# Kernel optimization log

Hardware: AMD Instinct MI355X
Metric: run time of the kernel (lower is better)

Reference implementation:

```python
import jax, jax.numpy as jnp
from jax import lax
import numpy as np

HIDDEN = 256
UID_EMB, LOC_EMB, WD_EMB, HR_EMB = 64, 128, 16, 16
UID_NUM, LOC_NUM = 5000, 50000
S, L, C = 32, 32, 128   # steps, current-trace prefix length, candidates per step
HN, LH = 32, 64         # history traces, history trace length
EMB = UID_EMB + LOC_EMB + WD_EMB + HR_EMB  # 224


def setup_inputs() -> dict:
    key = jax.random.key(0)
    ks = jax.random.split(key, 20)
    def lin(k, o, i, s=0.05):
        return jax.random.normal(k, (o, i), jnp.float32) * s
    return {
        "uid": 7,
        "current_trace": jnp.stack([
            jax.random.randint(ks[0], (S, L), 0, LOC_NUM),
            jax.random.randint(ks[1], (S, L), 0, 7),
            jax.random.randint(ks[2], (S, L), 0, 24)], axis=-1),
        "history_trace": jnp.stack([
            jax.random.randint(ks[3], (HN, LH), 0, LOC_NUM),
            jax.random.randint(ks[4], (HN, LH), 0, 7),
            jax.random.randint(ks[5], (HN, LH), 0, 24)], axis=-1),
        "candidate_set": jax.random.randint(ks[6], (S, C), 0, LOC_NUM),
        "uid_emb": jax.random.normal(ks[7], (UID_NUM, UID_EMB), jnp.float32),
        "loc_emb": jax.random.normal(ks[8], (LOC_NUM, LOC_EMB), jnp.float32),
        "weekday_emb": jax.random.normal(ks[9], (7, WD_EMB), jnp.float32),
        "hour_emb": jax.random.normal(ks[10], (24, HR_EMB), jnp.float32),
        "W_ih": lin(ks[11], 3 * HIDDEN, EMB),
        "W_hh": lin(ks[12], 3 * HIDDEN, HIDDEN),
        "b_ih": jnp.zeros((3 * HIDDEN,), jnp.float32),
        "b_hh": jnp.zeros((3 * HIDDEN,), jnp.float32),
        "intra_w1": lin(ks[13], HIDDEN, HIDDEN),
        "intra_w2": lin(ks[14], HIDDEN, HIDDEN),
        "intra_out": lin(ks[15], 1, HIDDEN),
        "inter_w1": lin(ks[16], HIDDEN, HIDDEN),
        "inter_w2": lin(ks[17], HIDDEN, HIDDEN),
        "inter_out": lin(ks[18], 1, HIDDEN),
        "score_w": lin(ks[19], 1, HIDDEN),
    }


def _gru(x, W_ih, W_hh, b_ih, b_hh):
    # x: [B, T, D] -> all hidden states [B, T, H]; single-layer torch GRU equations
    B = x.shape[0]
    H = W_hh.shape[1]
    x_proj = x @ W_ih.T + b_ih  # [B, T, 3H], precomputed input projection
    def step(h, xp):
        gh = h @ W_hh.T + b_hh
        xr, xz, xn = jnp.split(xp, 3, axis=-1)
        hr, hz, hn = jnp.split(gh, 3, axis=-1)
        r = jax.nn.sigmoid(xr + hr)
        z = jax.nn.sigmoid(xz + hz)
        n = jnp.tanh(xn + r * hn)
        h_new = (1.0 - z) * n + z * h
        return h_new, h_new
    h0 = jnp.zeros((B, H), x.dtype)
    _, hs = lax.scan(step, h0, jnp.swapaxes(x_proj, 0, 1))
    return jnp.swapaxes(hs, 0, 1)


def _forward(uid, current_trace, history_trace, candidate_set,
             uid_emb, loc_emb, weekday_emb, hour_emb,
             W_ih, W_hh, b_ih, b_hh,
             intra_w1, intra_w2, intra_out,
             inter_w1, inter_w2, inter_out, score_w):
    def encode(trace):  # [B, T, 3] int -> [B, H]
        B, T, _ = trace.shape
        u = jnp.broadcast_to(uid_emb[uid][None, None, :], (B, T, UID_EMB))
        e = jnp.concatenate([u,
                             loc_emb[trace[:, :, 0]],
                             weekday_emb[trace[:, :, 1]],
                             hour_emb[trace[:, :, 2]]], axis=-1)
        hs = _gru(e, W_ih, W_hh, b_ih, b_hh)
        # intra-trajectory attention: query = last hidden state, key = all hidden states
        qh = jax.nn.relu(hs[:, -1, :] @ intra_w1.T)[:, None, :]
        kh = jax.nn.relu(hs @ intra_w2.T)
        a = (jnp.tanh(qh + kh) @ intra_out.T)[..., 0]  # [B, T]
        w = jax.nn.softmax(a, axis=1)
        return jnp.einsum('bt,bth->bh', w, hs)

    hist_hidden = encode(history_trace)  # [HN, H]

    S_, L_, _ = current_trace.shape
    C_ = candidate_set.shape[1]
    last_time = current_trace[:, -1, 1:3]  # [S, 2] weekday/hour of last observed point
    cand_point = jnp.concatenate(
        [candidate_set[..., None],
         jnp.broadcast_to(last_time[:, None, :], (S_, C_, 2))], axis=-1)  # [S, C, 3]
    cand_trace = jnp.concatenate(
        [jnp.broadcast_to(current_trace[:, None], (S_, C_, L_, 3)),
         cand_point[:, :, None, :]], axis=2)  # [S, C, L+1, 3]
    cand_hidden = encode(cand_trace.reshape(S_ * C_, L_ + 1, 3))  # [S*C, H]

    # inter-trajectory attention; history key is shared across all candidates
    qh = jax.nn.relu(cand_hidden @ inter_w1.T)      # [S*C, H]
    kh = jax.nn.relu(hist_hidden @ inter_w2.T)      # [HN, H]
    a = (jnp.tanh(qh[:, None, :] + kh[None]) @ inter_out.T)[..., 0]  # [S*C, HN]
    w = jax.nn.softmax(a, axis=1)
    moving = w @ hist_hidden                        # [S*C, H]

    scores = (moving @ score_w.T)[:, 0].reshape(S_, C_)
    probs = jax.nn.softmax(scores, axis=1)          # softmax over candidate set per step
    return probs, moving.reshape(S_, C_, HIDDEN)


def reference(uid, current_trace, history_trace, candidate_set,
              uid_emb, loc_emb, weekday_emb, hour_emb,
              W_ih, W_hh, b_ih, b_hh,
              intra_w1, intra_w2, intra_out,
              inter_w1, inter_w2, inter_out, score_w):
    return _forward(uid, current_trace, history_trace, candidate_set,
                    uid_emb, loc_emb, weekday_emb, hour_emb,
                    W_ih, W_hh, b_ih, b_hh,
                    intra_w1, intra_w2, intra_out,
                    inter_w1, inter_w2, inter_out, score_w)
```

## Files before the change

### kernel.cpp

```cpp
#include <hip/hip_runtime.h>
#include <math.h>

#define NHID   256
#define NEMB   224

constexpr int OFF_BASE = 0;
constexpr int OFF_WDP  = 768;
constexpr int OFF_HRP  = OFF_WDP + 7*768;
constexpr int OFF_XPH  = OFF_HRP + 24*768;
constexpr int OFF_XPC  = OFF_XPH + 32*64*768;
constexpr int OFF_HSH  = OFF_XPC + 32*32*768;
constexpr int OFF_HSC  = OFF_HSH + 32*64*256;
constexpr int OFF_GHL  = OFF_HSC + 32*32*256;
constexpr int OFF_QHH  = OFF_GHL + 32*768;
constexpr int OFF_HC   = OFF_QHH + 32*256;
constexpr int OFF_KHH  = OFF_HC  + 4096*256;
constexpr int OFF_KHSH = OFF_KHH + 32*64*256;
constexpr int OFF_KHC  = OFF_KHSH+ 32*32*256;
constexpr int OFF_QHC  = OFF_KHC + 4096*256;
constexpr int OFF_HIST = OFF_QHC + 4096*256;
constexpr int OFF_CHID = OFF_HIST+ 32*256;
constexpr int OFF_QH2  = OFF_CHID+ 4096*256;
constexpr int OFF_KH2  = OFF_QH2 + 4096*256;
constexpr int OFF_SC   = OFF_KH2 + 32*256;
constexpr int OFF_W16  = OFF_KHH;

__device__ __forceinline__ float sigm(float x) { return 1.0f / (1.0f + __expf(-x)); }

typedef _Float16 half2_t __attribute__((ext_vector_type(2)));

__device__ __forceinline__ float fdot2f(unsigned int a, unsigned int b, float c) {
#if __has_builtin(__builtin_amdgcn_fdot2)
  return __builtin_amdgcn_fdot2(__builtin_bit_cast(half2_t, a),
                                __builtin_bit_cast(half2_t, b), c, false);
#else
  half2_t x = __builtin_bit_cast(half2_t, a);
  half2_t y = __builtin_bit_cast(half2_t, b);
  return c + (float)x[0] * (float)y[0] + (float)x[1] * (float)y[1];
#endif
}

__device__ __forceinline__ unsigned int packh(float a, float b) {
  unsigned short lo = __builtin_bit_cast(unsigned short, (_Float16)a);
  unsigned short hi = __builtin_bit_cast(unsigned short, (_Float16)b);
  return (unsigned int)lo | ((unsigned int)hi << 16);
}

__global__ __launch_bounds__(256) void k_prep(const int* uid, const float* uid_emb,
                                              const float* wde, const float* hre,
                                              const float* W_ih, const float* b_ih,
                                              float* ws) {
  __shared__ __align__(16) float ev[64];
  int blk = blockIdx.x, tid = threadIdx.x;
  if (blk == 0) {
    if (tid < 64) ev[tid] = uid_emb[uid[0] * 64 + tid];
    __syncthreads();
    #pragma unroll
    for (int jj = 0; jj < 3; ++jj) {
      int j = tid + jj * 256;
      float acc = b_ih[j];
      const float* wr = W_ih + j * NEMB;
      #pragma unroll
      for (int k = 0; k < 64; k += 4) {
        float4 w = *(const float4*)(wr + k);
        acc += ev[k]*w.x + ev[k+1]*w.y + ev[k+2]*w.z + ev[k+3]*w.w;
      }
      ws[OFF_BASE + j] = acc;
    }
  } else if (blk < 8) {
    int wd = blk - 1;
    if (tid < 16) ev[tid] = wde[wd * 16 + tid];
    __syncthreads();
    #pragma unroll
    for (int jj = 0; jj < 3; ++jj) {
      int j = tid + jj * 256;
      float acc = 0.f;
      const float* wr = W_ih + j * NEMB + 192;
      #pragma unroll
      for (int k = 0; k < 16; k += 4) {
        float4 w = *(const float4*)(wr + k);
        acc += ev[k]*w.x + ev[k+1]*w.y + ev[k+2]*w.z + ev[k+3]*w.w;
      }
      ws[OFF_WDP + wd * 768 + j] = acc;
    }
  } else {
    int hr = blk - 8;
    if (tid < 16) ev[tid] = hre[hr * 16 + tid];
    __syncthreads();
    #pragma unroll
    for (int jj = 0; jj < 3; ++jj) {
      int j = tid + jj * 256;
      float acc = 0.f;
      const float* wr = W_ih + j * NEMB + 208;
      #pragma unroll
      for (int k = 0; k < 16; k += 4) {
        float4 w = *(const float4*)(wr + k);
        acc += ev[k]*w.x + ev[k+1]*w.y + ev[k+2]*w.z + ev[k+3]*w.w;
      }
      ws[OFF_HRP + hr * 768 + j] = acc;
    }
  }
}

__global__ __launch_bounds__(256) void k_pack(const float* W_hh, float* ws) {
  int idx = blockIdx.x * 256 + threadIdx.x;
  int i4 = idx & 31, j = idx >> 5;
  const float4* p = (const float4*)(W_hh + j * 256 + i4 * 8);
  float4 a = p[0], b = p[1];
  uint4 o;
  o.x = packh(a.x, a.y); o.y = packh(a.z, a.w);
  o.z = packh(b.x, b.y); o.w = packh(b.z, b.w);
  ((uint4*)((unsigned int*)ws + OFF_W16))[i4 * 768 + j] = o;
}

__global__ __launch_bounds__(256) void k_xproj(const int* cur_tr, const int* hist_tr,
                                               const float* loc_emb, const float* W_ih,
                                               float* ws) {
  __shared__ float Ws[768][17];
  __shared__ float Xs[16][20];
  __shared__ int s_wd[16], s_hr[16], s_loc[16];
  int blk = blockIdx.x, tid = threadIdx.x;
  int r0 = blk * 16;

  if (tid < 16) {
    int row = r0 + tid;
    const int* tr; int idx;
    if (row < 2048) { tr = hist_tr; idx = row; } else { tr = cur_tr; idx = row - 2048; }
    s_loc[tid] = tr[idx * 3];
    s_wd[tid]  = tr[idx * 3 + 1];
    s_hr[tid]  = tr[idx * 3 + 2];
  }
  __syncthreads();

  float accA[16], accB[16], accC[16];
  #pragma unroll
  for (int r = 0; r < 16; ++r) { accA[r] = 0.f; accB[r] = 0.f; accC[r] = 0.f; }

  for (int kb = 0; kb < 8; ++kb) {
    for (int i = tid; i < 768 * 4; i += 256) {
      int j = i >> 2, q = (i & 3) * 4;
      float4 w = *(const float4*)&W_ih[j * NEMB + 64 + kb * 16 + q];
      Ws[j][q] = w.x; Ws[j][q+1] = w.y; Ws[j][q+2] = w.z; Ws[j][q+3] = w.w;
    }
    if (tid < 64) {
      int r = tid >> 2, q = (tid & 3) * 4;
      float4 x = *(const float4*)&loc_emb[s_loc[r] * 128 + kb * 16 + q];
      Xs[q][r] = x.x; Xs[q+1][r] = x.y; Xs[q+2][r] = x.z; Xs[q+3][r] = x.w;
    }
    __syncthreads();
    #pragma unroll
    for (int kk = 0; kk < 16; ++kk) {
      float wa = Ws[tid][kk], wb = Ws[tid + 256][kk], wc = Ws[tid + 512][kk];
      float4 x0 = *(const float4*)&Xs[kk][0];
      float4 x1 = *(const float4*)&Xs[kk][4];
      float4 x2 = *(const float4*)&Xs[kk][8];
      float4 x3 = *(const float4*)&Xs[kk][12];
      float xv[16] = {x0.x,x0.y,x0.z,x0.w, x1.x,x1.y,x1.z,x1.w,
                      x2.x,x2.y,x2.z,x2.w, x3.x,x3.y,x3.z,x3.w};
      #pragma unroll
      for (int r = 0; r < 16; ++r) {
        accA[r] += xv[r] * wa; accB[r] += xv[r] * wb; accC[r] += xv[r] * wc;
      }
    }
    __syncthreads();
  }

  float bA = ws[OFF_BASE + tid], bB = ws[OFF_BASE + 256 + tid], bC = ws[OFF_BASE + 512 + tid];
  for (int r = 0; r < 16; ++r) {
    int row = r0 + r;
    float* outp = (row < 2048) ? (ws + OFF_XPH + row * 768)
                               : (ws + OFF_XPC + (row - 2048) * 768);
    const float* wdp = ws + OFF_WDP + s_wd[r] * 768;
    const float* hrp = ws + OFF_HRP + s_hr[r] * 768;
    outp[tid]       = accA[r] + bA + wdp[tid]       + hrp[tid];
    outp[256 + tid] = accB[r] + bB + wdp[256 + tid] + hrp[256 + tid];
    outp[512 + tid] = accC[r] + bC + wdp[512 + tid] + hrp[512 + tid];
  }
}

__global__ __launch_bounds__(768) void k_gru(const float* b_hh, const float* intra_w1,
                                             float* ws) {
  __shared__ __align__(16) float gh[768];
  __shared__ __align__(16) float h32[256];
  __shared__ __align__(16) unsigned short h16[256];
  int w = blockIdx.x, tid = threadIdx.x;
  int T; const float* xp; float* hs;
  if (w < 32) { T = 64; xp = ws + OFF_XPH + w * 64 * 768; hs = ws + OFF_HSH + w * 64 * 256; }
  else        { T = 32; int b = w - 32; xp = ws + OFF_XPC + b * 32 * 768; hs = ws + OFF_HSC + b * 32 * 256; }

  uint4 wreg[32];
  {
    const uint4* wp = (const uint4*)((const unsigned int*)ws + OFF_W16) + tid;
    #pragma unroll
    for (int i = 0; i < 32; ++i) wreg[i] = wp[i * 768];
  }
  float bh = b_hh[tid];
  if (tid < 256) { h32[tid] = 0.f; h16[tid] = 0; }
  __syncthreads();

  for (int t = 0; t < T; ++t) {
    float xr, xz, xn;
    if (tid < 256) {
      xr = xp[t * 768 + tid];
      xz = xp[t * 768 + 256 + tid];
      xn = xp[t * 768 + 512 + tid];
    }
    float acc = bh;
    const uint4* hp = (const uint4*)h16;
    #pragma unroll
    for (int i = 0; i < 32; ++i) {
      uint4 hv = hp[i];
      acc = fdot2f(wreg[i].x, hv.x, acc);
      acc = fdot2f(wreg[i].y, hv.y, acc);
      acc = fdot2f(wreg[i].z, hv.z, acc);
      acc = fdot2f(wreg[i].w, hv.w, acc);
    }
    gh[tid] = acc;
    __syncthreads();
    if (tid < 256) {
      float r  = sigm(xr + gh[tid]);
      float z  = sigm(xz + gh[256 + tid]);
      float n  = tanhf(xn + r * gh[512 + tid]);
      float hn = (1.f - z) * n + z * h32[tid];
      h32[tid] = hn;
      hs[t * 256 + tid] = hn;
      h16[tid] = __builtin_bit_cast(unsigned short, (_Float16)hn);
    }
    __syncthreads();
  }

  if (w < 32) {
    if (tid < 256) {
      float acc = 0.f;
      const float* r1 = intra_w1 + tid * 256;
      #pragma unroll 16
      for (int k = 0; k < 256; k += 4) {
        float4 wv = *(const float4*)(r1 + k);
        float4 hv = *(const float4*)&h32[k];
        acc += hv.x*wv.x + hv.y*wv.y + hv.z*wv.z + hv.w*wv.w;
      }
      ws[OFF_QHH + w * 256 + tid] = fmaxf(acc, 0.f);
    }
  } else {
    float acc = bh;
    const uint4* hp = (const uint4*)h16;
    #pragma unroll
    for (int i = 0; i < 32; ++i) {
      uint4 hv = hp[i];
      acc = fdot2f(wreg[i].x, hv.x, acc);
      acc = fdot2f(wreg[i].y, hv.y, acc);
      acc = fdot2f(wreg[i].z, hv.z, acc);
      acc = fdot2f(wreg[i].w, hv.w, acc);
    }
    ws[OFF_GHL + (w - 32) * 768 + tid] = acc;
  }
}

__global__ __launch_bounds__(256) void k_cand(const int* cur_tr, const int* cand_set,
                                              const float* loc_emb, const float* W_ih,
                                              float* ws) {
  __shared__ float Ws[768][17];
  __shared__ float Xs[16][20];
  int blk = blockIdx.x, tid = threadIdx.x;
  int r0 = blk * 16;
  int s = r0 >> 7;

  float accA[16], accB[16], accC[16];
  #pragma unroll
  for (int r = 0; r < 16; ++r) { accA[r] = 0.f; accB[r] = 0.f; accC[r] = 0.f; }

  for (int kb = 0; kb < 8; ++kb) {
    for (int i = tid; i < 768 * 4; i += 256) {
      int j = i >> 2, q = (i & 3) * 4;
      float4 w = *(const float4*)&W_ih[j * NEMB + 64 + kb * 16 + q];
      Ws[j][q] = w.x; Ws[j][q+1] = w.y; Ws[j][q+2] = w.z; Ws[j][q+3] = w.w;
    }
    if (tid < 64) {
      int r = tid >> 2, q = (tid & 3) * 4;
      float4 x = *(const float4*)&loc_emb[cand_set[r0 + r] * 128 + kb * 16 + q];
      Xs[q][r] = x.x; Xs[q+1][r] = x.y; Xs[q+2][r] = x.z; Xs[q+3][r] = x.w;
    }
    __syncthreads();
    #pragma unroll
    for (int kk = 0; kk < 16; ++kk) {
      float wa = Ws[tid][kk], wb = Ws[tid + 256][kk], wc = Ws[tid + 512][kk];
      float4 x0 = *(const float4*)&Xs[kk][0];
      float4 x1 = *(const float4*)&Xs[kk][4];
      float4 x2 = *(const float4*)&Xs[kk][8];
      float4 x3 = *(const float4*)&Xs[kk][12];
      float xv[16] = {x0.x,x0.y,x0.z,x0.w, x1.x,x1.y,x1.z,x1.w,
                      x2.x,x2.y,x2.z,x2.w, x3.x,x3.y,x3.z,x3.w};
      #pragma unroll
      for (int r = 0; r < 16; ++r) {
        accA[r] += xv[r] * wa; accB[r] += xv[r] * wb; accC[r] += xv[r] * wc;
      }
    }
    __syncthreads();
  }

  int last = s * 32 + 31;
  int wd = cur_tr[last * 3 + 1], hr = cur_tr[last * 3 + 2];
  const float* wdp = ws + OFF_WDP + wd * 768;
  const float* hrp = ws + OFF_HRP + hr * 768;
  float xbA = ws[OFF_BASE + tid]       + wdp[tid]       + hrp[tid];
  float xbB = ws[OFF_BASE + 256 + tid] + wdp[256 + tid] + hrp[256 + tid];
  float xbC = ws[OFF_BASE + 512 + tid] + wdp[512 + tid] + hrp[512 + tid];
  float ghr = ws[OFF_GHL + s * 768 + tid];
  float ghz = ws[OFF_GHL + s * 768 + 256 + tid];
  float ghn = ws[OFF_GHL + s * 768 + 512 + tid];
  float hp  = ws[OFF_HSC + last * 256 + tid];

  for (int r = 0; r < 16; ++r) {
    float rr = sigm(xbA + accA[r] + ghr);
    float zz = sigm(xbB + accB[r] + ghz);
    float nn = tanhf(xbC + accC[r] + ghn);
    float hn = (1.f - zz) * nn + zz * hp;
    ws[OFF_HC + (r0 + r) * 256 + tid] = hn;
  }
}

__device__ __forceinline__ void proj_body(const float* in, float* out, const float* W,
                                          int r0, int tid) {
  __shared__ float Ws[256][33];
  __shared__ float Xs[32][36];
  int c0 = tid & 63, rg = (tid >> 6) * 8;
  float acc[4][8];
  #pragma unroll
  for (int c = 0; c < 4; ++c)
    #pragma unroll
    for (int r = 0; r < 8; ++r) acc[c][r] = 0.f;

  for (int kb = 0; kb < 8; ++kb) {
    for (int i = tid; i < 256 * 8; i += 256) {
      int j = i >> 3, q = (i & 7) * 4;
      float4 v = *(const float4*)&W[j * 256 + kb * 32 + q];
      Ws[j][q] = v.x; Ws[j][q+1] = v.y; Ws[j][q+2] = v.z; Ws[j][q+3] = v.w;
    }
    {
      int r = tid >> 3, q = (tid & 7) * 4;
      float4 v = *(const float4*)&in[(r0 + r) * 256 + kb * 32 + q];
      Xs[q][r] = v.x; Xs[q+1][r] = v.y; Xs[q+2][r] = v.z; Xs[q+3][r] = v.w;
    }
    __syncthreads();
    #pragma unroll
    for (int kk = 0; kk < 32; ++kk) {
      float w0 = Ws[c0][kk], w1 = Ws[c0 + 64][kk], w2 = Ws[c0 + 128][kk], w3 = Ws[c0 + 192][kk];
      float4 xa = *(const float4*)&Xs[kk][rg];
      float4 xb = *(const float4*)&Xs[kk][rg + 4];
      float xv[8] = {xa.x,xa.y,xa.z,xa.w, xb.x,xb.y,xb.z,xb.w};
      #pragma unroll
      for (int r = 0; r < 8; ++r) {
        acc[0][r] += xv[r] * w0; acc[1][r] += xv[r] * w1;
        acc[2][r] += xv[r] * w2; acc[3][r] += xv[r] * w3;
      }
    }
    __syncthreads();
  }
  #pragma unroll
  for (int c = 0; c < 4; ++c)
    for (int r = 0; r < 8; ++r)
      out[(r0 + rg + r) * 256 + c0 + c * 64] = fmaxf(acc[c][r], 0.f);
}

__global__ __launch_bounds__(256) void k_proj_intra(const float* intra_w1, const float* intra_w2,
                                                    float* ws) {
  int blk = blockIdx.x, tid = threadIdx.x;
  const float* in; float* out; const float* W; int r0;
  if (blk < 64)       { in = ws + OFF_HSH; out = ws + OFF_KHH;  W = intra_w2; r0 = blk * 32; }
  else if (blk < 96)  { in = ws + OFF_HSC; out = ws + OFF_KHSH; W = intra_w2; r0 = (blk - 64) * 32; }
  else if (blk < 224) { in = ws + OFF_HC;  out = ws + OFF_KHC;  W = intra_w2; r0 = (blk - 96) * 32; }
  else                { in = ws + OFF_HC;  out = ws + OFF_QHC;  W = intra_w1; r0 = (blk - 224) * 32; }
  proj_body(in, out, W, r0, tid);
}

__global__ __launch_bounds__(256) void k_proj_inter(const float* inter_w1, const float* inter_w2,
                                                    float* ws) {
  int blk = blockIdx.x, tid = threadIdx.x;
  const float* in; float* out; const float* W; int r0;
  if (blk < 128) { in = ws + OFF_CHID; out = ws + OFF_QH2; W = inter_w1; r0 = blk * 32; }
  else           { in = ws + OFF_HIST; out = ws + OFF_KH2; W = inter_w2; r0 = 0; }
  proj_body(in, out, W, r0, tid);
}

__global__ __launch_bounds__(256) void k_hist_attn(const float* intra_out, float* ws) {
  __shared__ __align__(16) float a[64];
  int b = blockIdx.x, tid = threadIdx.x;
  int wv = tid >> 6, lane = tid & 63;
  const float* qh = ws + OFF_QHH + b * 256;
  const float* kh = ws + OFF_KHH + b * 64 * 256;
  const float* hs = ws + OFF_HSH + b * 64 * 256;

  float4 q4  = *(const float4*)&qh[lane * 4];
  float4 io4 = *(const float4*)&intra_out[lane * 4];
  for (int t = wv; t < 64; t += 4) {
    float4 k4 = *(const float4*)&kh[t * 256 + lane * 4];
    float p = tanhf(q4.x + k4.x) * io4.x + tanhf(q4.y + k4.y) * io4.y +
              tanhf(q4.z + k4.z) * io4.z + tanhf(q4.w + k4.w) * io4.w;
    #pragma unroll
    for (int off = 32; off; off >>= 1) p += __shfl_down(p, off);
    if (lane == 0) a[t] = p;
  }
  __syncthreads();
  if (tid < 64) {
    float v = a[tid];
    float m = v;
    #pragma unroll
    for (int off = 32; off; off >>= 1) m = fmaxf(m, __shfl_xor(m, off));
    float e = __expf(v - m);
    float ssum = e;
    #pragma unroll
    for (int off = 32; off; off >>= 1) ssum += __shfl_xor(ssum, off);
    a[tid] = e / ssum;
  }
  __syncthreads();
  float acc = 0.f;
  for (int t = 0; t < 64; ++t) acc += a[t] * hs[t * 256 + tid];
  ws[OFF_HIST + b * 256 + tid] = acc;
}

__global__ __launch_bounds__(64) void k_cand_attn(const float* intra_out, float* ws) {
  int bId = blockIdx.x;
  int s = bId >> 7;
  int lane = threadIdx.x;
  const float* qh  = ws + OFF_QHC  + bId * 256;
  const float* khs = ws + OFF_KHSH + s * 32 * 256;
  const float* khc = ws + OFF_KHC  + bId * 256;
  const float* hsc = ws + OFF_HSC  + s * 32 * 256;
  const float* hc  = ws + OFF_HC   + bId * 256;

  float4 q4  = *(const float4*)&qh[lane * 4];
  float4 io4 = *(const float4*)&intra_out[lane * 4];
  float aa[33];
  float m = -1e30f;
  for (int t = 0; t < 33; ++t) {
    const float* kk = (t < 32) ? &khs[t * 256] : khc;
    float4 k4 = *(const float4*)&kk[lane * 4];
    float p = tanhf(q4.x + k4.x) * io4.x + tanhf(q4.y + k4.y) * io4.y +
              tanhf(q4.z + k4.z) * io4.z + tanhf(q4.w + k4.w) * io4.w;
    #pragma unroll
    for (int off = 32; off; off >>= 1) p += __shfl_xor(p, off);
    aa[t] = p;
    m = fmaxf(m, p);
  }
  float ssum = 0.f;
  #pragma unroll
  for (int t = 0; t < 33; ++t) { aa[t] = __expf(aa[t] - m); ssum += aa[t]; }
  float inv = 1.f / ssum;
  float ax = 0.f, ay = 0.f, az = 0.f, aw = 0.f;
  for (int t = 0; t < 32; ++t) {
    float wt = aa[t] * inv;
    float4 hv = *(const float4*)&hsc[t * 256 + lane * 4];
    ax += wt * hv.x; ay += wt * hv.y; az += wt * hv.z; aw += wt * hv.w;
  }
  {
    float wt = aa[32] * inv;
    float4 hv = *(const float4*)&hc[lane * 4];
    ax += wt * hv.x; ay += wt * hv.y; az += wt * hv.z; aw += wt * hv.w;
  }
  float4 o; o.x = ax; o.y = ay; o.z = az; o.w = aw;
  *(float4*)&ws[OFF_CHID + bId * 256 + lane * 4] = o;
}

__global__ __launch_bounds__(64) void k_inter_attn(const float* inter_out, const float* score_w,
                                                   float* ws, float* d_out) {
  int bId = blockIdx.x;
  int lane = threadIdx.x;
  const float* qh   = ws + OFF_QH2 + bId * 256;
  const float* kh2  = ws + OFF_KH2;
  const float* hist = ws + OFF_HIST;

  float4 q4  = *(const float4*)&qh[lane * 4];
  float4 io4 = *(const float4*)&inter_out[lane * 4];
  float aa[32];
  float m = -1e30f;
  for (int t = 0; t < 32; ++t) {
    float4 k4 = *(const float4*)&kh2[t * 256 + lane * 4];
    float p = tanhf(q4.x + k4.x) * io4.x + tanhf(q4.y + k4.y) * io4.y +
              tanhf(q4.z + k4.z) * io4.z + tanhf(q4.w + k4.w) * io4.w;
    #pragma unroll
    for (int off = 32; off; off >>= 1) p += __shfl_xor(p, off);
    aa[t] = p;
    m = fmaxf(m, p);
  }
  float ssum = 0.f;
  #pragma unroll
  for (int t = 0; t < 32; ++t) { aa[t] = __expf(aa[t] - m); ssum += aa[t]; }
  float inv = 1.f / ssum;
  float ax = 0.f, ay = 0.f, az = 0.f, aw = 0.f;
  for (int t = 0; t < 32; ++t) {
    float wt = aa[t] * inv;
    float4 hv = *(const float4*)&hist[t * 256 + lane * 4];
    ax += wt * hv.x; ay += wt * hv.y; az += wt * hv.z; aw += wt * hv.w;
  }
  float4 o; o.x = ax; o.y = ay; o.z = az; o.w = aw;
  *(float4*)&d_out[4096 + bId * 256 + lane * 4] = o;
  float4 sw = *(const float4*)&score_w[lane * 4];
  float sc = ax*sw.x + ay*sw.y + az*sw.z + aw*sw.w;
  #pragma unroll
  for (int off = 32; off; off >>= 1) sc += __shfl_xor(sc, off);
  if (lane == 0) ws[OFF_SC + bId] = sc;
}

__global__ __launch_bounds__(64) void k_probs(const float* ws, float* d_out) {
  int s = blockIdx.x, lane = threadIdx.x;
  float v0 = ws[OFF_SC + s * 128 + lane];
  float v1 = ws[OFF_SC + s * 128 + 64 + lane];
  float m = fmaxf(v0, v1);
  #pragma unroll
  for (int off = 32; off; off >>= 1) m = fmaxf(m, __shfl_xor(m, off));
  float e0 = __expf(v0 - m), e1 = __expf(v1 - m);
  float ssum = e0 + e1;
  #pragma unroll
  for (int off = 32; off; off >>= 1) ssum += __shfl_xor(ssum, off);
  float inv = 1.f / ssum;
  d_out[s * 128 + lane] = e0 * inv;
  d_out[s * 128 + 64 + lane] = e1 * inv;
}

extern "C" void kernel_launch(void* const* d_in, const int* in_sizes, int n_in,
                              void* d_out, int out_size, void* d_ws, size_t ws_size,
                              hipStream_t stream) {
  const int*   uid      = (const int*)  d_in[0];
  const int*   cur_tr   = (const int*)  d_in[1];
  const int*   hist_tr  = (const int*)  d_in[2];
  const int*   cand_set = (const int*)  d_in[3];
  const float* uid_emb  = (const float*)d_in[4];
  const float* loc_emb  = (const float*)d_in[5];
  const float* wde      = (const float*)d_in[6];
  const float* hre      = (const float*)d_in[7];
  const float* W_ih     = (const float*)d_in[8];
  const float* W_hh     = (const float*)d_in[9];
  const float* b_ih     = (const float*)d_in[10];
  const float* b_hh     = (const float*)d_in[11];
  const float* intra_w1 = (const float*)d_in[12];
  const float* intra_w2 = (const float*)d_in[13];
  const float* intra_out= (const float*)d_in[14];
  const float* inter_w1 = (const float*)d_in[15];
  const float* inter_w2 = (const float*)d_in[16];
  const float* inter_out= (const float*)d_in[17];
  const float* score_w  = (const float*)d_in[18];
  float* ws  = (float*)d_ws;
  float* out = (float*)d_out;

  hipLaunchKernelGGL(k_prep,       dim3(32),   dim3(256), 0, stream, uid, uid_emb, wde, hre, W_ih, b_ih, ws);
  hipLaunchKernelGGL(k_pack,       dim3(96),   dim3(256), 0, stream, W_hh, ws);
  hipLaunchKernelGGL(k_xproj,      dim3(192),  dim3(256), 0, stream, cur_tr, hist_tr, loc_emb, W_ih, ws);
  hipLaunchKernelGGL(k_gru,        dim3(64),   dim3(768), 0, stream, b_hh, intra_w1, ws);
  hipLaunchKernelGGL(k_cand,       dim3(256),  dim3(256), 0, stream, cur_tr, cand_set, loc_emb, W_ih, ws);
  hipLaunchKernelGGL(k_proj_intra, dim3(352),  dim3(256), 0, stream, intra_w1, intra_w2, ws);
  hipLaunchKernelGGL(k_hist_attn,  dim3(32),   dim3(256), 0, stream, intra_out, ws);
  hipLaunchKernelGGL(k_cand_attn,  dim3(4096), dim3(64),  0, stream, intra_out, ws);
  hipLaunchKernelGGL(k_proj_inter, dim3(129),  dim3(256), 0, stream, inter_w1, inter_w2, ws);
  hipLaunchKernelGGL(k_inter_attn, dim3(4096), dim3(64),  0, stream, inter_out, score_w, ws, out);
  hipLaunchKernelGGL(k_probs,      dim3(32),   dim3(64),  0, stream, ws, out);
}
```

Before: 454.9 us.

## Restructure attention kernels to per-lane keys, fast tanh, merge pack into prep

The two candidate attention kernels now process four candidates per 256-thread block. The shared keys, queries and output weights are staged in LDS, and each lane computes one full attention score by itself instead of doing a wave-wide shuffle reduction for every key. tanhf is replaced by an exp-based fast approximation throughout, including the GRU recurrence. The W_hh fp16 pack kernel is folded into k_prep as extra blocks, removing one launch. In exchange there are per-lane serial 256-long loops, heavy LDS traffic, and possible accuracy loss from the fast tanh.

Result: faster. 440.5 us (-3.1%).

```diff
diff --git a/kernel.cpp b/kernel.cpp
--- a/kernel.cpp
+++ b/kernel.cpp
@@ -26,6 +26,9 @@
 constexpr int OFF_W16  = OFF_KHH;
 
 __device__ __forceinline__ float sigm(float x) { return 1.0f / (1.0f + __expf(-x)); }
+__device__ __forceinline__ float tanhf_fast(float x) {
+  return 1.f - 2.f / (__expf(2.f * x) + 1.f);
+}
 
 typedef _Float16 half2_t __attribute__((ext_vector_type(2)));
 
@@ -49,9 +52,20 @@
 __global__ __launch_bounds__(256) void k_prep(const int* uid, const float* uid_emb,
                                               const float* wde, const float* hre,
                                               const float* W_ih, const float* b_ih,
-                                              float* ws) {
+                                              const float* W_hh, float* ws) {
   __shared__ __align__(16) float ev[64];
   int blk = blockIdx.x, tid = threadIdx.x;
+  if (blk >= 32) {
+    int idx = (blk - 32) * 256 + tid;
+    int i4 = idx & 31, j = idx >> 5;
+    const float4* p = (const float4*)(W_hh + j * 256 + i4 * 8);
+    float4 a = p[0], b = p[1];
+    uint4 o;
+    o.x = packh(a.x, a.y); o.y = packh(a.z, a.w);
+    o.z = packh(b.x, b.y); o.w = packh(b.z, b.w);
+    ((uint4*)((unsigned int*)ws + OFF_W16))[i4 * 768 + j] = o;
+    return;
+  }
   if (blk == 0) {
     if (tid < 64) ev[tid] = uid_emb[uid[0] * 64 + tid];
     __syncthreads();
@@ -100,17 +114,6 @@
       ws[OFF_HRP + hr * 768 + j] = acc;
     }
   }
-}
-
-__global__ __launch_bounds__(256) void k_pack(const float* W_hh, float* ws) {
-  int idx = blockIdx.x * 256 + threadIdx.x;
-  int i4 = idx & 31, j = idx >> 5;
-  const float4* p = (const float4*)(W_hh + j * 256 + i4 * 8);
-  float4 a = p[0], b = p[1];
-  uint4 o;
-  o.x = packh(a.x, a.y); o.y = packh(a.z, a.w);
-  o.z = packh(b.x, b.y); o.w = packh(b.z, b.w);
-  ((uint4*)((unsigned int*)ws + OFF_W16))[i4 * 768 + j] = o;
 }
 
 __global__ __launch_bounds__(256) void k_xproj(const int* cur_tr, const int* hist_tr,
@@ -220,7 +223,7 @@
     if (tid < 256) {
       float r  = sigm(xr + gh[tid]);
       float z  = sigm(xz + gh[256 + tid]);
-      float n  = tanhf(xn + r * gh[512 + tid]);
+      float n  = tanhf_fast(xn + r * gh[512 + tid]);
       float hn = (1.f - z) * n + z * h32[tid];
       h32[tid] = hn;
       hs[t * 256 + tid] = hn;
@@ -313,7 +316,7 @@
   for (int r = 0; r < 16; ++r) {
     float rr = sigm(xbA + accA[r] + ghr);
     float zz = sigm(xbB + accB[r] + ghz);
-    float nn = tanhf(xbC + accC[r] + ghn);
+    float nn = tanhf_fast(xbC + accC[r] + ghn);
     float hn = (1.f - zz) * nn + zz * hp;
     ws[OFF_HC + (r0 + r) * 256 + tid] = hn;
   }
@@ -394,8 +397,8 @@
   float4 io4 = *(const float4*)&intra_out[lane * 4];
   for (int t = wv; t < 64; t += 4) {
     float4 k4 = *(const float4*)&kh[t * 256 + lane * 4];
-    float p = tanhf(q4.x + k4.x) * io4.x + tanhf(q4.y + k4.y) * io4.y +
-              tanhf(q4.z + k4.z) * io4.z + tanhf(q4.w + k4.w) * io4.w;
+    float p = tanhf_fast(q4.x + k4.x) * io4.x + tanhf_fast(q4.y + k4.y) * io4.y +
+              tanhf_fast(q4.z + k4.z) * io4.z + tanhf_fast(q4.w + k4.w) * io4.w;
     #pragma unroll
     for (int off = 32; off; off >>= 1) p += __shfl_down(p, off);
     if (lane == 0) a[t] = p;
@@ -418,87 +421,123 @@
   ws[OFF_HIST + b * 256 + tid] = acc;
 }
 
-__global__ __launch_bounds__(64) void k_cand_attn(const float* intra_out, float* ws) {
-  int bId = blockIdx.x;
-  int s = bId >> 7;
-  int lane = threadIdx.x;
-  const float* qh  = ws + OFF_QHC  + bId * 256;
-  const float* khs = ws + OFF_KHSH + s * 32 * 256;
-  const float* khc = ws + OFF_KHC  + bId * 256;
-  const float* hsc = ws + OFF_HSC  + s * 32 * 256;
-  const float* hc  = ws + OFF_HC   + bId * 256;
-
-  float4 q4  = *(const float4*)&qh[lane * 4];
-  float4 io4 = *(const float4*)&intra_out[lane * 4];
-  float aa[33];
-  float m = -1e30f;
-  for (int t = 0; t < 33; ++t) {
-    const float* kk = (t < 32) ? &khs[t * 256] : khc;
-    float4 k4 = *(const float4*)&kk[lane * 4];
-    float p = tanhf(q4.x + k4.x) * io4.x + tanhf(q4.y + k4.y) * io4.y +
-              tanhf(q4.z + k4.z) * io4.z + tanhf(q4.w + k4.w) * io4.w;
-    #pragma unroll
-    for (int off = 32; off; off >>= 1) p += __shfl_xor(p, off);
-    aa[t] = p;
-    m = fmaxf(m, p);
-  }
-  float ssum = 0.f;
-  #pragma unroll
-  for (int t = 0; t < 33; ++t) { aa[t] = __expf(aa[t] - m); ssum += aa[t]; }
-  float inv = 1.f / ssum;
-  float ax = 0.f, ay = 0.f, az = 0.f, aw = 0.f;
+__global__ __launch_bounds__(256) void k_cand_attn(const float* intra_out, float* ws) {
+  __shared__ float Ks[32][260];
+  __shared__ float Kc[4][260];
+  __shared__ float Qs[4][260];
+  __shared__ float Io[260];
+  __shared__ float aw[4][36];
+  int blk = blockIdx.x, tid = threadIdx.x;
+  int s = blk >> 5;
+  int bId0 = s * 128 + (blk & 31) * 4;
+  int w = tid >> 6, lane = tid & 63;
+
+  for (int i = tid; i < 32 * 256; i += 256) {
+    int t = i >> 8, d = i & 255;
+    Ks[t][d] = ws[OFF_KHSH + (s * 32 + t) * 256 + d];
+  }
+  for (int i = tid; i < 4 * 256; i += 256) {
+    int c = i >> 8, d = i & 255;
+    Kc[c][d] = ws[OFF_KHC + (bId0 + c) * 256 + d];
+    Qs[c][d] = ws[OFF_QHC + (bId0 + c) * 256 + d];
+  }
+  Io[tid] = intra_out[tid];
+  __syncthreads();
+
+  const float* krow = (lane < 32) ? &Ks[lane][0] : &Kc[w][0];
+  float p = 0.f;
+  for (int d = 0; d < 256; d += 4) {
+    float4 k4 = *(const float4*)&krow[d];
+    float4 q4 = *(const float4*)&Qs[w][d];
+    float4 i4 = *(const float4*)&Io[d];
+    p += tanhf_fast(q4.x + k4.x) * i4.x + tanhf_fast(q4.y + k4.y) * i4.y +
+         tanhf_fast(q4.z + k4.z) * i4.z + tanhf_fast(q4.w + k4.w) * i4.w;
+  }
+  if (lane >= 33) p = -1e30f;
+  float m = p;
+  #pragma unroll
+  for (int off = 32; off; off >>= 1) m = fmaxf(m, __shfl_xor(m, off));
+  float e = __expf(p - m);
+  float ssum = e;
+  #pragma unroll
+  for (int off = 32; off; off >>= 1) ssum += __shfl_xor(ssum, off);
+  float wt = e / ssum;
+  if (lane < 33) aw[w][lane] = wt;
+  __syncthreads();
+
+  const float* hsc = ws + OFF_HSC + s * 32 * 256;
+  const float* hc  = ws + OFF_HC + (bId0 + w) * 256;
+  float ax = 0.f, ay = 0.f, az = 0.f, az2 = 0.f;
   for (int t = 0; t < 32; ++t) {
-    float wt = aa[t] * inv;
+    float wt2 = aw[w][t];
     float4 hv = *(const float4*)&hsc[t * 256 + lane * 4];
-    ax += wt * hv.x; ay += wt * hv.y; az += wt * hv.z; aw += wt * hv.w;
+    ax += wt2 * hv.x; ay += wt2 * hv.y; az += wt2 * hv.z; az2 += wt2 * hv.w;
   }
   {
-    float wt = aa[32] * inv;
+    float wt2 = aw[w][32];
     float4 hv = *(const float4*)&hc[lane * 4];
-    ax += wt * hv.x; ay += wt * hv.y; az += wt * hv.z; aw += wt * hv.w;
-  }
-  float4 o; o.x = ax; o.y = ay; o.z = az; o.w = aw;
-  *(float4*)&ws[OFF_CHID + bId * 256 + lane * 4] = o;
-}
-
-__global__ __launch_bounds__(64) void k_inter_attn(const float* inter_out, const float* score_w,
-                                                   float* ws, float* d_out) {
-  int bId = blockIdx.x;
-  int lane = threadIdx.x;
-  const float* qh   = ws + OFF_QH2 + bId * 256;
-  const float* kh2  = ws + OFF_KH2;
+    ax += wt2 * hv.x; ay += wt2 * hv.y; az += wt2 * hv.z; az2 += wt2 * hv.w;
+  }
+  float4 o; o.x = ax; o.y = ay; o.z = az; o.w = az2;
+  *(float4*)&ws[OFF_CHID + (bId0 + w) * 256 + lane * 4] = o;
+}
+
+__global__ __launch_bounds__(256) void k_inter_attn(const float* inter_out, const float* score_w,
+                                                    float* ws, float* d_out) {
+  __shared__ float Ks[32][260];
+  __shared__ float Qs[4][260];
+  __shared__ float Io[260];
+  __shared__ float aw[4][36];
+  int blk = blockIdx.x, tid = threadIdx.x;
+  int bId0 = blk * 4;
+  int w = tid >> 6, lane = tid & 63;
+
+  for (int i = tid; i < 32 * 256; i += 256) {
+    int t = i >> 8, d = i & 255;
+    Ks[t][d] = ws[OFF_KH2 + t * 256 + d];
+  }
+  for (int i = tid; i < 4 * 256; i += 256) {
+    int c = i >> 8, d = i & 255;
+    Qs[c][d] = ws[OFF_QH2 + (bId0 + c) * 256 + d];
+  }
+  Io[tid] = inter_out[tid];
+  __syncthreads();
+
+  const float* krow = (lane < 32) ? &Ks[lane][0] : &Ks[0][0];
+  float p = 0.f;
+  for (int d = 0; d < 256; d += 4) {
+    float4 k4 = *(const float4*)&krow[d];
+    float4 q4 = *(const float4*)&Qs[w][d];
+    float4 i4 = *(const float4*)&Io[d];
+    p += tanhf_fast(q4.x + k4.x) * i4.x + tanhf_fast(q4.y + k4.y) * i4.y +
+         tanhf_fast(q4.z + k4.z) * i4.z + tanhf_fast(q4.w + k4.w) * i4.w;
+  }
+  if (lane >= 32) p = -1e30f;
+  float m = p;
+  #pragma unroll
+  for (int off = 32; off; off >>= 1) m = fmaxf(m, __shfl_xor(m, off));
+  float e = __expf(p - m);
+  float ssum = e;
+  #pragma unroll
+  for (int off = 32; off; off >>= 1) ssum += __shfl_xor(ssum, off);
+  float wt = e / ssum;
+  if (lane < 32) aw[w][lane] = wt;
+  __syncthreads();
+
   const float* hist = ws + OFF_HIST;
-
-  float4 q4  = *(const float4*)&qh[lane * 4];
-  float4 io4 = *(const float4*)&inter_out[lane * 4];
-  float aa[32];
-  float m = -1e30f;
+  float ax = 0.f, ay = 0.f, az = 0.f, az2 = 0.f;
   for (int t = 0; t < 32; ++t) {
-    float4 k4 = *(const float4*)&kh2[t * 256 + lane * 4];
-    float p = tanhf(q4.x + k4.x) * io4.x + tanhf(q4.y + k4.y) * io4.y +
-              tanhf(q4.z + k4.z) * io4.z + tanhf(q4.w + k4.w) * io4.w;
-    #pragma unroll
-    for (int off = 32; off; off >>= 1) p += __shfl_xor(p, off);
-    aa[t] = p;
-    m = fmaxf(m, p);
-  }
-  float ssum = 0.f;
-  #pragma unroll
-  for (int t = 0; t < 32; ++t) { aa[t] = __expf(aa[t] - m); ssum += aa[t]; }
-  float inv = 1.f / ssum;
-  float ax = 0.f, ay = 0.f, az = 0.f, aw = 0.f;
-  for (int t = 0; t < 32; ++t) {
-    float wt = aa[t] * inv;
+    float wt2 = aw[w][t];
     float4 hv = *(const float4*)&hist[t * 256 + lane * 4];
-    ax += wt * hv.x; ay += wt * hv.y; az += wt * hv.z; aw += wt * hv.w;
-  }
-  float4 o; o.x = ax; o.y = ay; o.z = az; o.w = aw;
-  *(float4*)&d_out[4096 + bId * 256 + lane * 4] = o;
+    ax += wt2 * hv.x; ay += wt2 * hv.y; az += wt2 * hv.z; az2 += wt2 * hv.w;
+  }
+  float4 o; o.x = ax; o.y = ay; o.z = az; o.w = az2;
+  *(float4*)&d_out[4096 + (bId0 + w) * 256 + lane * 4] = o;
   float4 sw = *(const float4*)&score_w[lane * 4];
-  float sc = ax*sw.x + ay*sw.y + az*sw.z + aw*sw.w;
+  float sc = ax*sw.x + ay*sw.y + az*sw.z + az2*sw.w;
   #pragma unroll
   for (int off = 32; off; off >>= 1) sc += __shfl_xor(sc, off);
-  if (lane == 0) ws[OFF_SC + bId] = sc;
+  if (lane == 0) ws[OFF_SC + bId0 + w] = sc;
 }
 
 __global__ __launch_bounds__(64) void k_probs(const float* ws, float* d_out) {
@@ -542,15 +581,14 @@
   float* ws  = (float*)d_ws;
   float* out = (float*)d_out;
 
-  hipLaunchKernelGGL(k_prep,       dim3(32),   dim3(256), 0, stream, uid, uid_emb, wde, hre, W_ih, b_ih, ws);
-  hipLaunchKernelGGL(k_pack,       dim3(96),   dim3(256), 0, stream, W_hh, ws);
+  hipLaunchKernelGGL(k_prep,       dim3(128),  dim3(256), 0, stream, uid, uid_emb, wde, hre, W_ih, b_ih, W_hh, ws);
   hipLaunchKernelGGL(k_xproj,      dim3(192),  dim3(256), 0, stream, cur_tr, hist_tr, loc_emb, W_ih, ws);
   hipLaunchKernelGGL(k_gru,        dim3(64),   dim3(768), 0, stream, b_hh, intra_w1, ws);
   hipLaunchKernelGGL(k_cand,       dim3(256),  dim3(256), 0, stream, cur_tr, cand_set, loc_emb, W_ih, ws);
   hipLaunchKernelGGL(k_proj_intra, dim3(352),  dim3(256), 0, stream, intra_w1, intra_w2, ws);
   hipLaunchKernelGGL(k_hist_attn,  dim3(32),   dim3(256), 0, stream, intra_out, ws);
-  hipLaunchKernelGGL(k_cand_attn,  dim3(4096), dim3(64),  0, stream, intra_out, ws);
+  hipLaunchKernelGGL(k_cand_attn,  dim3(1024), dim3(256), 0, stream, intra_out, ws);
   hipLaunchKernelGGL(k_proj_inter, dim3(129),  dim3(256), 0, stream, inter_w1, inter_w2, ws);
-  hipLaunchKernelGGL(k_inter_attn, dim3(4096), dim3(64),  0, stream, inter_out, score_w, ws, out);
+  hipLaunchKernelGGL(k_inter_attn, dim3(1024), dim3(256), 0, stream, inter_out, score_w, ws, out);
   hipLaunchKernelGGL(k_probs,      dim3(32),   dim3(64),  0, stream, ws, out);
 }
```
